# Kernel tuning notes

Measured on AMD Instinct MI355X. Metric: run time of the kernel, lower is better.

## Reference

```python
import jax, jax.numpy as jnp
import numpy as np
import math

B, S, D, H = 4, 2048, 768, 12
DK = D // H

def setup_inputs() -> dict:
    key = jax.random.key(0)
    ks = jax.random.split(key, 12)
    sc = 1.0 / math.sqrt(D)
    return {
        'Q': jax.random.normal(ks[0], (B, S, D), jnp.float32),
        'K': jax.random.normal(ks[1], (B, S, D), jnp.float32),
        'V': jax.random.normal(ks[2], (B, S, D), jnp.float32),
        'mask': jax.random.randint(ks[3], (B, 1, S, S), 0, 2, jnp.int32),
        'Wq': jax.random.normal(ks[4], (D, D), jnp.float32) * sc,
        'bq': jnp.zeros((D,), jnp.float32),
        'Wk': jax.random.normal(ks[5], (D, D), jnp.float32) * sc,
        'bk': jnp.zeros((D,), jnp.float32),
        'Wv': jax.random.normal(ks[6], (D, D), jnp.float32) * sc,
        'bv': jnp.zeros((D,), jnp.float32),
        'Wo': jax.random.normal(ks[7], (D, D), jnp.float32) * sc,
        'bo': jnp.zeros((D,), jnp.float32),
    }

def _split_heads(x):
    # [B,S,D] -> [B,H,S,DK]
    return x.reshape(B, S, H, DK).transpose(0, 2, 1, 3)

def reference(Q, K, V, mask, Wq, bq, Wk, bk, Wv, bv, Wo, bo):
    q = _split_heads(Q @ Wq.T + bq)
    k = _split_heads(K @ Wk.T + bk)
    v = _split_heads(V @ Wv.T + bv)
    scores = jnp.einsum('bhqd,bhkd->bhqk', q, k) / math.sqrt(DK)
    # Faithful to the source: masked positions are filled with -1e-9 (NOT -inf)
    scores = jnp.where(mask == 0, jnp.float32(-1e-9), scores)
    attn = jax.nn.softmax(scores, axis=-1)
    x = jnp.einsum('bhqk,bhkd->bhqd', attn, v)          # [B,H,S,DK]
    x = x.transpose(0, 2, 1, 3).reshape(B, S, D)         # [B,S,D]
    return x @ Wo.T + bo
```

## Files before the change

kernel.cpp:

```cpp
#include <hip/hip_runtime.h>

#define BB 4
#define SS 2048
#define DD 768
#define HH 12
#define DKK 64
#define MM (BB*SS)

typedef __attribute__((ext_vector_type(8))) short bf16x8;
typedef __attribute__((ext_vector_type(4))) float f32x4;

#define GLDS(g, l) __builtin_amdgcn_global_load_lds( \
    (const __attribute__((address_space(1))) unsigned int*)(g), \
    (__attribute__((address_space(3))) unsigned int*)(l), 16, 0, 0)

__device__ __forceinline__ unsigned short f2bf(float f) {
    union { float f; unsigned int u; } v; v.f = f;
    unsigned int r = v.u + 0x7fffu + ((v.u >> 16) & 1u);
    return (unsigned short)(r >> 16);
}

#define EXPSCALE 0.18033688011112042f

#define NACT4 (MM*DD/4)
#define ABLK  (NACT4/256)
#define NW4   (DD*DD/4)
#define WBLK  (NW4/256)
#define MBLK  (BB*SS*SS/256)

__global__ void prep(
    const float* __restrict__ Q, const float* __restrict__ K, const float* __restrict__ V,
    const float* __restrict__ Wq, const float* __restrict__ Wk, const float* __restrict__ Wv,
    const float* __restrict__ Wo, const int* __restrict__ mask,
    unsigned short* __restrict__ Qc, unsigned short* __restrict__ Kc, unsigned short* __restrict__ Vc,
    unsigned short* __restrict__ Wqc, unsigned short* __restrict__ Wkc, unsigned short* __restrict__ Wvc,
    unsigned short* __restrict__ Woc, unsigned int* __restrict__ mbits)
{
    const int bx = blockIdx.x;
    if (bx < 3 * ABLK) {
        const int seg = bx / ABLK;
        const float* s = seg == 0 ? Q : seg == 1 ? K : V;
        unsigned short* d = seg == 0 ? Qc : seg == 1 ? Kc : Vc;
        const int i = (bx - seg * ABLK) * 256 + threadIdx.x;
        float4 v = ((const float4*)s)[i];
        ushort4 o;
        o.x = f2bf(v.x); o.y = f2bf(v.y); o.z = f2bf(v.z); o.w = f2bf(v.w);
        ((ushort4*)d)[i] = o;
    } else if (bx < 3 * ABLK + 4 * WBLK) {
        const int b2 = bx - 3 * ABLK;
        const int seg = b2 / WBLK;
        const float* s = seg == 0 ? Wq : seg == 1 ? Wk : seg == 2 ? Wv : Wo;
        unsigned short* d = seg == 0 ? Wqc : seg == 1 ? Wkc : seg == 2 ? Wvc : Woc;
        const int i = (b2 - seg * WBLK) * 256 + threadIdx.x;
        float4 v = ((const float4*)s)[i];
        ushort4 o;
        o.x = f2bf(v.x); o.y = f2bf(v.y); o.z = f2bf(v.z); o.w = f2bf(v.w);
        ((ushort4*)d)[i] = o;
    } else {
        const int t = (bx - (3 * ABLK + 4 * WBLK)) * 256 + threadIdx.x;
        const int m = mask[t];
        unsigned long long b = __ballot(m != 0);
        const int l = t & 63;
        if (l == 0)       mbits[t >> 5] = (unsigned int)b;
        else if (l == 32) mbits[t >> 5] = (unsigned int)(b >> 32);
    }
}

__global__ __launch_bounds__(256) void gemm_qkv(
    const unsigned short* __restrict__ Qc, const unsigned short* __restrict__ Kc, const unsigned short* __restrict__ Vc,
    const unsigned short* __restrict__ Wq, const unsigned short* __restrict__ Wk, const unsigned short* __restrict__ Wv,
    const float* __restrict__ bq, const float* __restrict__ bk, const float* __restrict__ bv,
    unsigned short* __restrict__ qb, unsigned short* __restrict__ kb, unsigned short* __restrict__ vt)
{
    __shared__ unsigned short As[128*64];
    __shared__ unsigned short Bs[128*64];
    const int mat = blockIdx.z;
    const unsigned short* X = mat == 0 ? Qc : mat == 1 ? Kc : Vc;
    const unsigned short* W = mat == 0 ? Wq : mat == 1 ? Wk : Wv;
    const float* bias        = mat == 0 ? bq : mat == 1 ? bk : bv;

    const int tid  = threadIdx.x;
    const int lane = tid & 63;
    const int w    = tid >> 6;
    const int wm   = w >> 1, wn = w & 1;
    const int quad = lane >> 4, c = lane & 15;
    const int m0 = blockIdx.y * 128, n0 = blockIdx.x * 128;

    f32x4 acc[4][4];
    #pragma unroll
    for (int i = 0; i < 4; i++)
        #pragma unroll
        for (int j = 0; j < 4; j++) acc[i][j] = (f32x4){0.f, 0.f, 0.f, 0.f};

    const unsigned short* Xg[4]; const unsigned short* Wg[4]; int dst[4];
    #pragma unroll
    for (int j = 0; j < 4; j++) {
        const int ch = tid + j * 256;
        const int row = ch >> 3, sl = ch & 7;
        const int lc = (sl ^ (row & 7)) << 3;
        Xg[j] = X + (size_t)(m0 + row) * DD + lc;
        Wg[j] = W + (size_t)(n0 + row) * DD + lc;
        dst[j] = ch * 8;
    }
    const int cswz = c & 7;

    for (int k0 = 0; k0 < DD; k0 += 64) {
        #pragma unroll
        for (int j = 0; j < 4; j++) {
            GLDS(Xg[j] + k0, As + dst[j]);
            GLDS(Wg[j] + k0, Bs + dst[j]);
        }
        __syncthreads();
        #pragma unroll
        for (int kk = 0; kk < 2; kk++) {
            bf16x8 a[4], b[4];
            #pragma unroll
            for (int t = 0; t < 4; t++) {
                const int ra = wm * 64 + t * 16 + c;
                const int rb = wn * 64 + t * 16 + c;
                a[t] = *(const bf16x8*)(As + ra * 64 + (((kk * 4 + quad) ^ cswz) << 3));
                b[t] = *(const bf16x8*)(Bs + rb * 64 + (((kk * 4 + quad) ^ cswz) << 3));
            }
            if (mat < 2) {
                #pragma unroll
                for (int tn = 0; tn < 4; tn++)
                    #pragma unroll
                    for (int tm = 0; tm < 4; tm++)
                        acc[tn][tm] = __builtin_amdgcn_mfma_f32_16x16x32_bf16(b[tn], a[tm], acc[tn][tm], 0, 0, 0);
            } else {
                #pragma unroll
                for (int tm = 0; tm < 4; tm++)
                    #pragma unroll
                    for (int tn = 0; tn < 4; tn++)
                        acc[tm][tn] = __builtin_amdgcn_mfma_f32_16x16x32_bf16(a[tm], b[tn], acc[tm][tn], 0, 0, 0);
            }
        }
        __syncthreads();
    }

    if (mat < 2) {
        unsigned short* out = mat == 0 ? qb : kb;
        const float scale = mat == 0 ? EXPSCALE : 1.0f;
        #pragma unroll
        for (int tn = 0; tn < 4; tn++) {
            const int featbase = n0 + wn * 64 + tn * 16 + quad * 4;
            const float4 bz = *(const float4*)(bias + featbase);
            #pragma unroll
            for (int tm = 0; tm < 4; tm++) {
                const int token = m0 + wm * 64 + tm * 16 + c;
                ushort4 pk;
                pk.x = f2bf((acc[tn][tm][0] + bz.x) * scale);
                pk.y = f2bf((acc[tn][tm][1] + bz.y) * scale);
                pk.z = f2bf((acc[tn][tm][2] + bz.z) * scale);
                pk.w = f2bf((acc[tn][tm][3] + bz.w) * scale);
                *(ushort4*)(out + (size_t)token * DD + featbase) = pk;
            }
        }
    } else {
        #pragma unroll
        for (int tn = 0; tn < 4; tn++) {
            const int col = n0 + wn * 64 + tn * 16 + c;
            const float bz = bias[col];
            const int h = col >> 6, dk = col & 63;
            #pragma unroll
            for (int tm = 0; tm < 4; tm++) {
                const int row = m0 + wm * 64 + tm * 16 + quad * 4;
                const int bb = row >> 11, s = row & 2047;
                ushort4 pk;
                pk.x = f2bf(acc[tm][tn][0] + bz);
                pk.y = f2bf(acc[tm][tn][1] + bz);
                pk.z = f2bf(acc[tm][tn][2] + bz);
                pk.w = f2bf(acc[tm][tn][3] + bz);
                *(ushort4*)(vt + ((((size_t)bb * HH + h) * DKK + dk) * SS + s)) = pk;
            }
        }
    }
}

__global__ __launch_bounds__(256, 3) void flash(
    const unsigned short* __restrict__ qb, const unsigned short* __restrict__ kb,
    const unsigned short* __restrict__ vt, const unsigned int* __restrict__ mbits,
    unsigned short* __restrict__ ob)
{
    __shared__ unsigned short Ks[2][64*64];
    __shared__ unsigned short Vs[2][64*64];

    const int bh = blockIdx.y;
    const int bi = bh / HH, h = bh % HH;
    const int tid  = threadIdx.x;
    const int w    = tid >> 6, lane = tid & 63;
    const int quad = lane >> 4, c = lane & 15;
    const int q0w = blockIdx.x * 128 + w * 32;

    bf16x8 qa[2][2];
    #pragma unroll
    for (int mt = 0; mt < 2; mt++) {
        const unsigned short* qbase = qb + (size_t)(bi * SS + q0w + mt * 16 + c) * DD + h * DKK + quad * 8;
        qa[mt][0] = *(const bf16x8*)(qbase);
        qa[mt][1] = *(const bf16x8*)(qbase + 32);
    }

    const int l0 = tid >> 3, sl = tid & 7;
    const int l1 = 32 + l0;
    const int lc = (sl ^ (l0 & 7)) << 3;
    const int kp0 = ((l0 >> 5) << 5) | (((l0 >> 2) & 3) << 3) | (((l0 >> 4) & 1) << 2) | (l0 & 3);
    const int kp1 = ((l1 >> 5) << 5) | (((l1 >> 2) & 3) << 3) | (((l1 >> 4) & 1) << 2) | (l1 & 3);
    const unsigned short* kg0 = kb + ((size_t)bi * SS + kp0) * DD + h * DKK + lc;
    const unsigned short* kg1 = kb + ((size_t)bi * SS + kp1) * DD + h * DKK + lc;
    const unsigned short* vg0 = vt + (((size_t)bi * HH + h) * DKK + l0) * SS + lc;
    const unsigned short* vg1 = vt + (((size_t)bi * HH + h) * DKK + l1) * SS + lc;

    const unsigned int* mrow0 = mbits + (size_t)(bi * SS + q0w + c) * (SS / 32);
    const unsigned int* mrow1 = mrow0 + (size_t)16 * (SS / 32);

    f32x4 o[2][4];
    #pragma unroll
    for (int mt = 0; mt < 2; mt++)
        #pragma unroll
        for (int dt = 0; dt < 4; dt++) o[mt][dt] = (f32x4){0.f, 0.f, 0.f, 0.f};
    f32x4 osum[2] = { (f32x4){0.f,0.f,0.f,0.f}, (f32x4){0.f,0.f,0.f,0.f} };
    const f32x4 ZC = (f32x4){0.f, 0.f, 0.f, 0.f};
    union { unsigned int u[4]; bf16x8 v; } onesu;
    onesu.u[0] = 0x3F803F80u; onesu.u[1] = 0x3F803F80u;
    onesu.u[2] = 0x3F803F80u; onesu.u[3] = 0x3F803F80u;
    const bf16x8 ones = onesu.v;

    const int cswz = c & 7;

    GLDS(kg0, Ks[0] + (size_t)tid * 8);
    GLDS(kg1, Ks[0] + (size_t)(256 + tid) * 8);
    GLDS(vg0, Vs[0] + (size_t)tid * 8);
    GLDS(vg1, Vs[0] + (size_t)(256 + tid) * 8);
    uint2 mw0 = *(const uint2*)(mrow0);
    uint2 mw1 = *(const uint2*)(mrow1);

    for (int t = 0; t < SS / 64; t++) {
        const int k0 = t * 64, par = t & 1;
        __syncthreads();
        uint2 nw0 = make_uint2(0u, 0u), nw1 = make_uint2(0u, 0u);
        if (t < SS / 64 - 1) {
            const size_t ko = (size_t)(k0 + 64);
            GLDS(kg0 + ko * DD, Ks[par ^ 1] + (size_t)tid * 8);
            GLDS(kg1 + ko * DD, Ks[par ^ 1] + (size_t)(256 + tid) * 8);
            GLDS(vg0 + ko,      Vs[par ^ 1] + (size_t)tid * 8);
            GLDS(vg1 + ko,      Vs[par ^ 1] + (size_t)(256 + tid) * 8);
            nw0 = *(const uint2*)(mrow0 + ((k0 + 64) >> 5));
            nw1 = *(const uint2*)(mrow1 + ((k0 + 64) >> 5));
        }

        const unsigned long long mmq[2] = {
            ((((unsigned long long)mw0.y << 32) | mw0.x) >> (quad * 8)),
            ((((unsigned long long)mw1.y << 32) | mw1.x) >> (quad * 8)) };

        #pragma unroll
        for (int p = 0; p < 2; p++) {
            unsigned int pq[2][4];
            #pragma unroll
            for (int tt = 0; tt < 2; tt++) {
                const unsigned short* kbase = &Ks[par][((2 * p + tt) * 16 + c) << 6];
                const bf16x8 kf0 = *(const bf16x8*)(kbase + ((quad ^ cswz) << 3));
                const bf16x8 kf1 = *(const bf16x8*)(kbase + (((4 + quad) ^ cswz) << 3));
                #pragma unroll
                for (int mt = 0; mt < 2; mt++) {
                    f32x4 st = __builtin_amdgcn_mfma_f32_16x16x32_bf16(kf0, qa[mt][0], ZC, 0, 0, 0);
                    st = __builtin_amdgcn_mfma_f32_16x16x32_bf16(kf1, qa[mt][1], st, 0, 0, 0);
                    const unsigned int mb = (unsigned int)(mmq[mt] >> (p * 32 + tt * 4)) & 15u;
                    #pragma unroll
                    for (int r2 = 0; r2 < 2; r2++) {
                        const float sv0 = (mb & (1u << (r2 * 2)))     ? st[r2 * 2]     : 0.0f;
                        const float sv1 = (mb & (1u << (r2 * 2 + 1))) ? st[r2 * 2 + 1] : 0.0f;
                        const float p0 = __builtin_amdgcn_exp2f(sv0);
                        const float p1 = __builtin_amdgcn_exp2f(sv1);
                        union { float f; unsigned int u; } u0, u1; u0.f = p0; u1.f = p1;
                        pq[mt][tt * 2 + r2] = __builtin_amdgcn_perm(u1.u, u0.u, 0x07060302);
                    }
                }
            }
            bf16x8 pbv[2];
            #pragma unroll
            for (int mt = 0; mt < 2; mt++) {
                union { unsigned int u[4]; bf16x8 v; } pb;
                pb.u[0] = pq[mt][0]; pb.u[1] = pq[mt][1];
                pb.u[2] = pq[mt][2]; pb.u[3] = pq[mt][3];
                pbv[mt] = pb.v;
                osum[mt] = __builtin_amdgcn_mfma_f32_16x16x32_bf16(ones, pbv[mt], osum[mt], 0, 0, 0);
            }
            #pragma unroll
            for (int dt = 0; dt < 4; dt++) {
                const bf16x8 vf = *(const bf16x8*)(&Vs[par][((dt * 16 + c) << 6) + ((((p << 2) + quad) ^ cswz) << 3)]);
                #pragma unroll
                for (int mt = 0; mt < 2; mt++)
                    o[mt][dt] = __builtin_amdgcn_mfma_f32_16x16x32_bf16(vf, pbv[mt], o[mt][dt], 0, 0, 0);
            }
        }
        mw0 = nw0; mw1 = nw1;
    }

    #pragma unroll
    for (int mt = 0; mt < 2; mt++) {
        const float rn = __builtin_amdgcn_rcpf(osum[mt][0]);
        unsigned short* op = ob + (size_t)(bi * SS + q0w + mt * 16 + c) * DD + h * DKK + quad * 4;
        #pragma unroll
        for (int dt = 0; dt < 4; dt++) {
            ushort4 pk;
            pk.x = f2bf(o[mt][dt][0] * rn);
            pk.y = f2bf(o[mt][dt][1] * rn);
            pk.z = f2bf(o[mt][dt][2] * rn);
            pk.w = f2bf(o[mt][dt][3] * rn);
            *(ushort4*)(op + dt * 16) = pk;
        }
    }
}

__global__ __launch_bounds__(256) void gemm_out(
    const unsigned short* __restrict__ A, const unsigned short* __restrict__ W,
    const float* __restrict__ bias, float* __restrict__ out)
{
    __shared__ unsigned short As[128*64];
    __shared__ unsigned short Bs[128*64];
    const int tid  = threadIdx.x;
    const int lane = tid & 63;
    const int w    = tid >> 6;
    const int wm   = w >> 1, wn = w & 1;
    const int quad = lane >> 4, c = lane & 15;
    const int m0 = blockIdx.y * 128, n0 = blockIdx.x * 128;

    f32x4 acc[4][4];
    #pragma unroll
    for (int i = 0; i < 4; i++)
        #pragma unroll
        for (int j = 0; j < 4; j++) acc[i][j] = (f32x4){0.f, 0.f, 0.f, 0.f};

    const unsigned short* Ag[4]; const unsigned short* Wg[4]; int dst[4];
    #pragma unroll
    for (int j = 0; j < 4; j++) {
        const int ch = tid + j * 256;
        const int row = ch >> 3, sl = ch & 7;
        const int lcc = (sl ^ (row & 7)) << 3;
        Ag[j] = A + (size_t)(m0 + row) * DD + lcc;
        Wg[j] = W + (size_t)(n0 + row) * DD + lcc;
        dst[j] = ch * 8;
    }
    const int cswz = c & 7;

    for (int k0 = 0; k0 < DD; k0 += 64) {
        #pragma unroll
        for (int j = 0; j < 4; j++) {
            GLDS(Ag[j] + k0, As + dst[j]);
            GLDS(Wg[j] + k0, Bs + dst[j]);
        }
        __syncthreads();
        #pragma unroll
        for (int kk = 0; kk < 2; kk++) {
            bf16x8 a[4], b[4];
            #pragma unroll
            for (int t = 0; t < 4; t++) {
                const int ra = wm * 64 + t * 16 + c;
                const int rb = wn * 64 + t * 16 + c;
                a[t] = *(const bf16x8*)(As + ra * 64 + (((kk * 4 + quad) ^ cswz) << 3));
                b[t] = *(const bf16x8*)(Bs + rb * 64 + (((kk * 4 + quad) ^ cswz) << 3));
            }
            #pragma unroll
            for (int tn = 0; tn < 4; tn++)
                #pragma unroll
                for (int tm = 0; tm < 4; tm++)
                    acc[tn][tm] = __builtin_amdgcn_mfma_f32_16x16x32_bf16(b[tn], a[tm], acc[tn][tm], 0, 0, 0);
        }
        __syncthreads();
    }

    #pragma unroll
    for (int tn = 0; tn < 4; tn++) {
        const int featbase = n0 + wn * 64 + tn * 16 + quad * 4;
        const float4 bz = *(const float4*)(bias + featbase);
        #pragma unroll
        for (int tm = 0; tm < 4; tm++) {
            const int token = m0 + wm * 64 + tm * 16 + c;
            float4 v;
            v.x = acc[tn][tm][0] + bz.x;
            v.y = acc[tn][tm][1] + bz.y;
            v.z = acc[tn][tm][2] + bz.z;
            v.w = acc[tn][tm][3] + bz.w;
            *(float4*)(out + (size_t)token * DD + featbase) = v;
        }
    }
}

extern "C" void kernel_launch(void* const* d_in, const int* in_sizes, int n_in,
                              void* d_out, int out_size, void* d_ws, size_t ws_size,
                              hipStream_t stream) {
    (void)in_sizes; (void)n_in; (void)out_size; (void)ws_size;
    const float* Q    = (const float*)d_in[0];
    const float* K    = (const float*)d_in[1];
    const float* V    = (const float*)d_in[2];
    const int*   mask = (const int*)d_in[3];
    const float* Wq   = (const float*)d_in[4];
    const float* bq   = (const float*)d_in[5];
    const float* Wk   = (const float*)d_in[6];
    const float* bk   = (const float*)d_in[7];
    const float* Wv   = (const float*)d_in[8];
    const float* bv   = (const float*)d_in[9];
    const float* Wo   = (const float*)d_in[10];
    const float* bo   = (const float*)d_in[11];
    float* out = (float*)d_out;

    char* ws = (char*)d_ws;
    size_t off = 0;
    auto alloc = [&](size_t bytes) { char* p = ws + off; off += (bytes + 255) & ~255ULL; return p; };
    const size_t act = (size_t)MM * DD * 2;
    unsigned short* Qc  = (unsigned short*)alloc(act);
    unsigned short* Kc  = (unsigned short*)alloc(act);
    unsigned short* Vc  = (unsigned short*)alloc(act);
    unsigned short* Wqc = (unsigned short*)alloc((size_t)DD * DD * 2);
    unsigned short* Wkc = (unsigned short*)alloc((size_t)DD * DD * 2);
    unsigned short* Wvc = (unsigned short*)alloc((size_t)DD * DD * 2);
    unsigned short* Woc = (unsigned short*)alloc((size_t)DD * DD * 2);
    unsigned short* qb  = (unsigned short*)alloc(act);
    unsigned short* kb  = (unsigned short*)alloc(act);
    unsigned short* vt  = (unsigned short*)alloc(act);
    unsigned int*  mbits = (unsigned int*)alloc((size_t)BB * SS * (SS / 32) * 4);
    unsigned short* ob = Qc;

    prep<<<dim3(3 * ABLK + 4 * WBLK + MBLK), 256, 0, stream>>>(
        Q, K, V, Wq, Wk, Wv, Wo, mask, Qc, Kc, Vc, Wqc, Wkc, Wvc, Woc, mbits);
    gemm_qkv<<<dim3(DD / 128, MM / 128, 3), 256, 0, stream>>>(
        Qc, Kc, Vc, Wqc, Wkc, Wvc, bq, bk, bv, qb, kb, vt);
    flash<<<dim3(SS / 128, BB * HH), 256, 0, stream>>>(qb, kb, vt, mbits, ob);
    gemm_out<<<dim3(DD / 128, MM / 128), 256, 0, stream>>>(ob, Woc, bo, out);
}
```

Baseline: 358.4 us.

## Vectorize mask bit-packing, widen prep work per thread, swizzle GEMM blocks across XCDs

The prep kernel now reads the int32 mask with 16-byte loads and builds four ballots per wave, writing a permuted bit layout. The flash kernel reads that layout with 128-bit loads once every four key tiles and extracts bits per tile. The fp32-to-bf16 conversion handles two vectors per thread. Both GEMMs use a 1-D grid remapped so that consecutive blocks sharing an M tile land on the same XCD, aiming for better L2 reuse. The goal is to cut the bandwidth and instruction cost of the mask pass and improve cache locality, at the cost of more bit-manipulation work inside the attention loop.

```diff
diff --git a/kernel.cpp b/kernel.cpp
--- a/kernel.cpp
+++ b/kernel.cpp
@@ -22,11 +22,11 @@
 
 #define EXPSCALE 0.18033688011112042f
 
-#define NACT4 (MM*DD/4)
-#define ABLK  (NACT4/256)
-#define NW4   (DD*DD/4)
-#define WBLK  (NW4/256)
-#define MBLK  (BB*SS*SS/256)
+#define ABLK2 (MM*DD/4/512)
+#define WBLK2 (DD*DD/4/512)
+#define MBLK2 (BB*SS*SS/1024)
+#define SEGW  (3*ABLK2)
+#define SEGM  (SEGW + 4*WBLK2)
 
 __global__ void prep(
     const float* __restrict__ Q, const float* __restrict__ K, const float* __restrict__ V,
@@ -37,32 +37,50 @@
     unsigned short* __restrict__ Woc, unsigned int* __restrict__ mbits)
 {
     const int bx = blockIdx.x;
-    if (bx < 3 * ABLK) {
-        const int seg = bx / ABLK;
+    if (bx < SEGW) {
+        const int seg = bx / ABLK2;
         const float* s = seg == 0 ? Q : seg == 1 ? K : V;
         unsigned short* d = seg == 0 ? Qc : seg == 1 ? Kc : Vc;
-        const int i = (bx - seg * ABLK) * 256 + threadIdx.x;
-        float4 v = ((const float4*)s)[i];
-        ushort4 o;
-        o.x = f2bf(v.x); o.y = f2bf(v.y); o.z = f2bf(v.z); o.w = f2bf(v.w);
-        ((ushort4*)d)[i] = o;
-    } else if (bx < 3 * ABLK + 4 * WBLK) {
-        const int b2 = bx - 3 * ABLK;
-        const int seg = b2 / WBLK;
+        const int i0 = (bx - seg * ABLK2) * 512 + threadIdx.x;
+        #pragma unroll
+        for (int j = 0; j < 2; j++) {
+            const int i = i0 + j * 256;
+            float4 v = ((const float4*)s)[i];
+            ushort4 o;
+            o.x = f2bf(v.x); o.y = f2bf(v.y); o.z = f2bf(v.z); o.w = f2bf(v.w);
+            ((ushort4*)d)[i] = o;
+        }
+    } else if (bx < SEGM) {
+        const int b2 = bx - SEGW;
+        const int seg = b2 / WBLK2;
         const float* s = seg == 0 ? Wq : seg == 1 ? Wk : seg == 2 ? Wv : Wo;
         unsigned short* d = seg == 0 ? Wqc : seg == 1 ? Wkc : seg == 2 ? Wvc : Woc;
-        const int i = (b2 - seg * WBLK) * 256 + threadIdx.x;
-        float4 v = ((const float4*)s)[i];
-        ushort4 o;
-        o.x = f2bf(v.x); o.y = f2bf(v.y); o.z = f2bf(v.z); o.w = f2bf(v.w);
-        ((ushort4*)d)[i] = o;
+        const int i0 = (b2 - seg * WBLK2) * 512 + threadIdx.x;
+        #pragma unroll
+        for (int j = 0; j < 2; j++) {
+            const int i = i0 + j * 256;
+            float4 v = ((const float4*)s)[i];
+            ushort4 o;
+            o.x = f2bf(v.x); o.y = f2bf(v.y); o.z = f2bf(v.z); o.w = f2bf(v.w);
+            ((ushort4*)d)[i] = o;
+        }
     } else {
-        const int t = (bx - (3 * ABLK + 4 * WBLK)) * 256 + threadIdx.x;
-        const int m = mask[t];
-        unsigned long long b = __ballot(m != 0);
-        const int l = t & 63;
-        if (l == 0)       mbits[t >> 5] = (unsigned int)b;
-        else if (l == 32) mbits[t >> 5] = (unsigned int)(b >> 32);
+        const int blk = bx - SEGM;
+        const int chunk = blk * 4 + (threadIdx.x >> 6);
+        const int l = threadIdx.x & 63;
+        const int4 mv = *(const int4*)(mask + (size_t)chunk * 256 + 4 * l);
+        const unsigned int nib = (mv.x != 0 ? 1u : 0u) | (mv.y != 0 ? 2u : 0u) |
+                                 (mv.z != 0 ? 4u : 0u) | (mv.w != 0 ? 8u : 0u);
+        const unsigned long long b0 = __ballot(nib & 1u);
+        const unsigned long long b1 = __ballot(nib & 2u);
+        const unsigned long long b2 = __ballot(nib & 4u);
+        const unsigned long long b3 = __ballot(nib & 8u);
+        if (l < 8) {
+            const int i = l >> 1;
+            const unsigned long long wsel = i == 0 ? b0 : i == 1 ? b1 : i == 2 ? b2 : b3;
+            const unsigned int v = (l & 1) ? (unsigned int)(wsel >> 32) : (unsigned int)wsel;
+            mbits[(size_t)chunk * 8 + l] = v;
+        }
     }
 }
 
@@ -74,7 +92,15 @@
 {
     __shared__ unsigned short As[128*64];
     __shared__ unsigned short Bs[128*64];
-    const int mat = blockIdx.z;
+    const int bid = blockIdx.x;
+    const int xg  = bid & 7;
+    const int s   = bid >> 3;
+    const int mat = s / 48;
+    const int r   = s % 48;
+    const int nb  = r % 6;
+    const int mb  = (r / 6) * 8 + xg;
+    const int m0 = mb * 128, n0 = nb * 128;
+
     const unsigned short* X = mat == 0 ? Qc : mat == 1 ? Kc : Vc;
     const unsigned short* W = mat == 0 ? Wq : mat == 1 ? Wk : Wv;
     const float* bias        = mat == 0 ? bq : mat == 1 ? bk : bv;
@@ -84,7 +110,6 @@
     const int w    = tid >> 6;
     const int wm   = w >> 1, wn = w & 1;
     const int quad = lane >> 4, c = lane & 15;
-    const int m0 = blockIdx.y * 128, n0 = blockIdx.x * 128;
 
     f32x4 acc[4][4];
     #pragma unroll
@@ -165,13 +190,13 @@
             #pragma unroll
             for (int tm = 0; tm < 4; tm++) {
                 const int row = m0 + wm * 64 + tm * 16 + quad * 4;
-                const int bb = row >> 11, s = row & 2047;
+                const int bb = row >> 11, ss = row & 2047;
                 ushort4 pk;
                 pk.x = f2bf(acc[tm][tn][0] + bz);
                 pk.y = f2bf(acc[tm][tn][1] + bz);
                 pk.z = f2bf(acc[tm][tn][2] + bz);
                 pk.w = f2bf(acc[tm][tn][3] + bz);
-                *(ushort4*)(vt + ((((size_t)bb * HH + h) * DKK + dk) * SS + s)) = pk;
+                *(ushort4*)(vt + ((((size_t)bb * HH + h) * DKK + dk) * SS + ss)) = pk;
             }
         }
     }
@@ -210,8 +235,8 @@
     const unsigned short* vg0 = vt + (((size_t)bi * HH + h) * DKK + l0) * SS + lc;
     const unsigned short* vg1 = vt + (((size_t)bi * HH + h) * DKK + l1) * SS + lc;
 
-    const unsigned int* mrow0 = mbits + (size_t)(bi * SS + q0w + c) * (SS / 32);
-    const unsigned int* mrow1 = mrow0 + (size_t)16 * (SS / 32);
+    const unsigned int* mr0 = mbits + (size_t)(bi * SS + q0w + c) * 64;
+    const unsigned int* mr1 = mr0 + (size_t)16 * 64;
 
     f32x4 o[2][4];
     #pragma unroll
@@ -231,26 +256,36 @@
     GLDS(kg1, Ks[0] + (size_t)(256 + tid) * 8);
     GLDS(vg0, Vs[0] + (size_t)tid * 8);
     GLDS(vg1, Vs[0] + (size_t)(256 + tid) * 8);
-    uint2 mw0 = *(const uint2*)(mrow0);
-    uint2 mw1 = *(const uint2*)(mrow1);
+
+    uint4 wlo[2], whi[2];
 
     for (int t = 0; t < SS / 64; t++) {
         const int k0 = t * 64, par = t & 1;
         __syncthreads();
-        uint2 nw0 = make_uint2(0u, 0u), nw1 = make_uint2(0u, 0u);
         if (t < SS / 64 - 1) {
             const size_t ko = (size_t)(k0 + 64);
             GLDS(kg0 + ko * DD, Ks[par ^ 1] + (size_t)tid * 8);
             GLDS(kg1 + ko * DD, Ks[par ^ 1] + (size_t)(256 + tid) * 8);
             GLDS(vg0 + ko,      Vs[par ^ 1] + (size_t)tid * 8);
             GLDS(vg1 + ko,      Vs[par ^ 1] + (size_t)(256 + tid) * 8);
-            nw0 = *(const uint2*)(mrow0 + ((k0 + 64) >> 5));
-            nw1 = *(const uint2*)(mrow1 + ((k0 + 64) >> 5));
-        }
-
-        const unsigned long long mmq[2] = {
-            ((((unsigned long long)mw0.y << 32) | mw0.x) >> (quad * 8)),
-            ((((unsigned long long)mw1.y << 32) | mw1.x) >> (quad * 8)) };
+        }
+
+        if ((t & 3) == 0) {
+            const int co = (t >> 2) * 8;
+            wlo[0] = *(const uint4*)(mr0 + co);
+            whi[0] = *(const uint4*)(mr0 + co + 4);
+            wlo[1] = *(const uint4*)(mr1 + co);
+            whi[1] = *(const uint4*)(mr1 + co + 4);
+        }
+        const int t16 = (t & 3) * 16;
+        unsigned int ww[2][4];
+        #pragma unroll
+        for (int mt = 0; mt < 2; mt++) {
+            ww[mt][0] = (unsigned int)((((unsigned long long)wlo[mt].y << 32) | wlo[mt].x) >> t16);
+            ww[mt][1] = (unsigned int)((((unsigned long long)wlo[mt].w << 32) | wlo[mt].z) >> t16);
+            ww[mt][2] = (unsigned int)((((unsigned long long)whi[mt].y << 32) | whi[mt].x) >> t16);
+            ww[mt][3] = (unsigned int)((((unsigned long long)whi[mt].w << 32) | whi[mt].z) >> t16);
+        }
 
         #pragma unroll
         for (int p = 0; p < 2; p++) {
@@ -260,15 +295,15 @@
                 const unsigned short* kbase = &Ks[par][((2 * p + tt) * 16 + c) << 6];
                 const bf16x8 kf0 = *(const bf16x8*)(kbase + ((quad ^ cswz) << 3));
                 const bf16x8 kf1 = *(const bf16x8*)(kbase + (((4 + quad) ^ cswz) << 3));
+                const unsigned int sh = (unsigned)(p * 8 + quad * 2 + tt);
                 #pragma unroll
                 for (int mt = 0; mt < 2; mt++) {
                     f32x4 st = __builtin_amdgcn_mfma_f32_16x16x32_bf16(kf0, qa[mt][0], ZC, 0, 0, 0);
                     st = __builtin_amdgcn_mfma_f32_16x16x32_bf16(kf1, qa[mt][1], st, 0, 0, 0);
-                    const unsigned int mb = (unsigned int)(mmq[mt] >> (p * 32 + tt * 4)) & 15u;
                     #pragma unroll
                     for (int r2 = 0; r2 < 2; r2++) {
-                        const float sv0 = (mb & (1u << (r2 * 2)))     ? st[r2 * 2]     : 0.0f;
-                        const float sv1 = (mb & (1u << (r2 * 2 + 1))) ? st[r2 * 2 + 1] : 0.0f;
+                        const float sv0 = ((ww[mt][r2 * 2]     >> sh) & 1u) ? st[r2 * 2]     : 0.0f;
+                        const float sv1 = ((ww[mt][r2 * 2 + 1] >> sh) & 1u) ? st[r2 * 2 + 1] : 0.0f;
                         const float p0 = __builtin_amdgcn_exp2f(sv0);
                         const float p1 = __builtin_amdgcn_exp2f(sv1);
                         union { float f; unsigned int u; } u0, u1; u0.f = p0; u1.f = p1;
@@ -293,7 +328,6 @@
                     o[mt][dt] = __builtin_amdgcn_mfma_f32_16x16x32_bf16(vf, pbv[mt], o[mt][dt], 0, 0, 0);
             }
         }
-        mw0 = nw0; mw1 = nw1;
     }
 
     #pragma unroll
@@ -318,12 +352,18 @@
 {
     __shared__ unsigned short As[128*64];
     __shared__ unsigned short Bs[128*64];
+    const int bid = blockIdx.x;
+    const int xg  = bid & 7;
+    const int s   = bid >> 3;
+    const int nb  = s % 6;
+    const int mb  = (s / 6) * 8 + xg;
+    const int m0 = mb * 128, n0 = nb * 128;
+
     const int tid  = threadIdx.x;
     const int lane = tid & 63;
     const int w    = tid >> 6;
     const int wm   = w >> 1, wn = w & 1;
     const int quad = lane >> 4, c = lane & 15;
-    const int m0 = blockIdx.y * 128, n0 = blockIdx.x * 128;
 
     f32x4 acc[4][4];
     #pragma unroll
@@ -421,10 +461,10 @@
     unsigned int*  mbits = (unsigned int*)alloc((size_t)BB * SS * (SS / 32) * 4);
     unsigned short* ob = Qc;
 
-    prep<<<dim3(3 * ABLK + 4 * WBLK + MBLK), 256, 0, stream>>>(
+    prep<<<dim3(SEGM + MBLK2), 256, 0, stream>>>(
         Q, K, V, Wq, Wk, Wv, Wo, mask, Qc, Kc, Vc, Wqc, Wkc, Wvc, Woc, mbits);
-    gemm_qkv<<<dim3(DD / 128, MM / 128, 3), 256, 0, stream>>>(
+    gemm_qkv<<<dim3(1152), 256, 0, stream>>>(
         Qc, Kc, Vc, Wqc, Wkc, Wvc, bq, bk, bv, qb, kb, vt);
     flash<<<dim3(SS / 128, BB * HH), 256, 0, stream>>>(qb, kb, vt, mbits, ob);
-    gemm_out<<<dim3(DD / 128, MM / 128), 256, 0, stream>>>(ob, Woc, bo, out);
-}
+    gemm_out<<<dim3(384), 256, 0, stream>>>(ob, Woc, bo, out);
+}
```

After: 321.5 us. 10.3% less time.
